# Performance work log

Measured on AMD Instinct MI355X. Metric: run time of the kernel, lower is better.

## Reference

```python
import jax, jax.numpy as jnp
import numpy as np

DIM = 256
HEADS = 8
HEAD_DIM = DIM // HEADS
B_, N = 8192, 49


def setup_inputs() -> dict:
    key = jax.random.key(0)
    k1, k2, k3, k4, k5, k6 = jax.random.split(key, 6)
    x = jax.random.normal(k1, (B_, N, DIM), dtype=jnp.float32)
    mask = jax.random.normal(k2, (B_, N, N), dtype=jnp.float32)
    s = 1.0 / np.sqrt(DIM)
    W_qkv = jax.random.normal(k3, (3 * DIM, DIM), dtype=jnp.float32) * s
    b_qkv = jax.random.normal(k4, (3 * DIM,), dtype=jnp.float32) * 0.02
    W_proj = jax.random.normal(k5, (DIM, DIM), dtype=jnp.float32) * s
    b_proj = jax.random.normal(k6, (DIM,), dtype=jnp.float32) * 0.02
    return {"x": x, "mask": mask, "W_qkv": W_qkv, "b_qkv": b_qkv,
            "W_proj": W_proj, "b_proj": b_proj}


def reference(x, mask, W_qkv, b_qkv, W_proj, b_proj):
    B, n, C = x.shape
    scale = HEAD_DIM ** (-0.5)
    # qkv projection: (B, N, 3C) -> (3, B, H, N, hd)
    qkv = x @ W_qkv.T + b_qkv
    qkv = qkv.reshape(B, n, 3, HEADS, HEAD_DIM).transpose(2, 0, 3, 1, 4)
    q, k, v = qkv[0], qkv[1], qkv[2]
    # scaled dot-product within each window
    attn = jnp.einsum('bhqd,bhkd->bhqk', q, k) * scale
    attn = attn + mask[:, None, :, :]  # additive window mask
    attn = jax.nn.softmax(attn, axis=-1)
    out = jnp.einsum('bhqk,bhkd->bhqd', attn, v)
    out = out.transpose(0, 2, 1, 3).reshape(B, n, C)
    return out @ W_proj.T + b_proj
```

## Files before the change

### kernel.cpp

```cpp
#include <hip/hip_runtime.h>
#include <hip/hip_bf16.h>

#define NTOK 49
#define DIMC 256

typedef __attribute__((ext_vector_type(8))) short bf16x8;
typedef __attribute__((ext_vector_type(4))) float f32x4;

static __device__ __forceinline__ unsigned pk2(float a, float b) {
    union { __hip_bfloat16 h; unsigned short u; } ua, ub;
    ua.h = __float2bfloat16(a);
    ub.h = __float2bfloat16(b);
    return (unsigned)ua.u | ((unsigned)ub.u << 16);
}

static __device__ __forceinline__ bf16x8 mkfrag(unsigned w0, unsigned w1, unsigned w2, unsigned w3) {
    union { bf16x8 v; unsigned u[4]; } t;
    t.u[0] = w0; t.u[1] = w1; t.u[2] = w2; t.u[3] = w3;
    return t.v;
}

static __device__ __forceinline__ unsigned sel2(unsigned lo, unsigned hi, int src, int ghi) {
    unsigned a = __shfl(lo, src);
    unsigned b = __shfl(hi, src);
    return ghi ? b : a;
}

__global__ void convert_weights(const float* __restrict__ wq, const float* __restrict__ wp,
                                unsigned short* __restrict__ wqb, unsigned short* __restrict__ wpb) {
    int i = blockIdx.x * 256 + threadIdx.x;
    if (i < 768 * 256) {
        union { __hip_bfloat16 h; unsigned short u; } t;
        t.h = __float2bfloat16(wq[i]);
        wqb[i] = t.u;
    }
    if (i < 256 * 256) {
        union { __hip_bfloat16 h; unsigned short u; } t;
        t.h = __float2bfloat16(wp[i]);
        wpb[i] = t.u;
    }
}

__launch_bounds__(512, 4)
__attribute__((amdgpu_waves_per_eu(4, 4)))
__global__ void win_attn_fused(const float* __restrict__ x, const float* __restrict__ mask,
                               const unsigned short* __restrict__ wqkv, const float* __restrict__ bqkv,
                               const unsigned short* __restrict__ wproj, const float* __restrict__ bproj,
                               float* __restrict__ out) {
    __shared__ __align__(16) char lds[81920];
    char* const xb  = lds;
    char* const kqv = lds + 32768;

    const int b = blockIdx.x;
    const int tid = threadIdx.x;
    const int lane = tid & 63;
    const int wid = tid >> 6;
    const int c = lane & 15;
    const int g = lane >> 4;
    const int lh = wid >> 1;
    const int qh = wid & 1;
    const int srcA = c + 16 * ((2 * g) & 3);
    const int srcB = c + 16 * ((2 * g + 1) & 3);
    const int ghi = g >> 1;
    const float scale = 0.17677669529663687f;
    const f32x4 fzero = {0.f, 0.f, 0.f, 0.f};

    char* const Kh = kqv + lh * 12288;
    char* const Qh = Kh + 4096;
    char* const Vh = Kh + 8192;

    {
        const float* xw = x + (size_t)b * (NTOK * DIMC);
        #pragma unroll
        for (int it = 0; it < 8; ++it) {
            int idx = it * 512 + tid;
            int t = idx >> 6;
            int d0 = (idx & 63) * 4;
            float4 v = make_float4(0.f, 0.f, 0.f, 0.f);
            if (t < NTOK) v = *(const float4*)(xw + t * DIMC + d0);
            *(uint2*)(xb + t * 512 + ((d0 * 2) ^ ((t & 7) << 4))) =
                make_uint2(pk2(v.x, v.y), pk2(v.z, v.w));
        }
    }
    __syncthreads();

    #define XFR(base_, t_, kk_) \
        (*(const bf16x8*)((base_) + (t_) * 512 + ((2 * ((kk_) + 8 * g)) ^ (((t_) & 7) << 4))))

    unsigned aout[2][2][2][2];

    #pragma unroll
    for (int r = 0; r < 2; ++r) {
        const int h = r * 4 + lh;

        {
            f32x4 aKQ[2][4], aV[4];
            #pragma unroll
            for (int md = 0; md < 2; ++md)
                #pragma unroll
                for (int j2 = 0; j2 < 4; ++j2) aKQ[md][j2] = fzero;
            #pragma unroll
            for (int mt = 0; mt < 4; ++mt) aV[mt] = fzero;

            const int woff = qh ? (h * 32) : (256 + h * 32);
            const unsigned short* wkq_base = wqkv + (size_t)(woff + c) * 256 + 8 * g;
            const unsigned short* wv_base  = wqkv + (size_t)(512 + h * 32 + qh * 16 + c) * 256 + 8 * g;
            #pragma unroll
            for (int ks = 0; ks < 8; ++ks) {
                int kk = ks * 32;
                bf16x8 xf[4];
                #pragma unroll
                for (int tt = 0; tt < 4; ++tt) { int t = tt * 16 + c; xf[tt] = XFR(xb, t, kk); }
                bf16x8 wkq0 = *(const bf16x8*)(wkq_base + kk);
                bf16x8 wkq1 = *(const bf16x8*)(wkq_base + 16 * 256 + kk);
                bf16x8 wv   = *(const bf16x8*)(wv_base + kk);
                #pragma unroll
                for (int j2 = 0; j2 < 4; ++j2) {
                    aKQ[0][j2] = __builtin_amdgcn_mfma_f32_16x16x32_bf16(wkq0, xf[j2], aKQ[0][j2], 0, 0, 0);
                    aKQ[1][j2] = __builtin_amdgcn_mfma_f32_16x16x32_bf16(wkq1, xf[j2], aKQ[1][j2], 0, 0, 0);
                    aV[j2]     = __builtin_amdgcn_mfma_f32_16x16x32_bf16(xf[j2], wv, aV[j2], 0, 0, 0);
                }
            }

            char* kqdst = (qh ? Qh : Kh);
            const float* bb = bqkv + (qh ? 0 : 256) + h * 32;
            #pragma unroll
            for (int md = 0; md < 2; ++md) {
                const float* b4 = bb + md * 16 + 4 * g;
                float b0 = b4[0], b1 = b4[1], b2 = b4[2], b3 = b4[3];
                #pragma unroll
                for (int j2 = 0; j2 < 4; ++j2) {
                    int t = j2 * 16 + c;
                    int d0 = md * 16 + 4 * g;
                    f32x4 v = aKQ[md][j2];
                    float v0 = v[0] + b0, v1 = v[1] + b1, v2 = v[2] + b2, v3 = v[3] + b3;
                    if (qh) { v0 *= scale; v1 *= scale; v2 *= scale; v3 *= scale; }
                    *(uint2*)(kqdst + t * 64 + ((d0 * 2) ^ ((t & 3) << 4))) =
                        make_uint2(pk2(v0, v1), pk2(v2, v3));
                }
            }
            float bv = bqkv[512 + h * 32 + qh * 16 + c];
            #pragma unroll
            for (int mt = 0; mt < 4; ++mt) {
                int t0 = mt * 16 + 4 * g;
                int d = qh * 16 + c;
                f32x4 v = aV[mt];
                *(uint2*)(Vh + d * 128 + ((t0 * 2) ^ ((d & 7) << 4))) =
                    make_uint2(pk2(v[0] + bv, v[1] + bv), pk2(v[2] + bv, v[3] + bv));
            }
        }
        __syncthreads();

        {
            const float* mw = mask + (size_t)b * (NTOK * NTOK);
            f32x4 mv[2][3];
            float m48[2];
            #pragma unroll
            for (int jl = 0; jl < 2; ++jl) {
                int q = (qh * 2 + jl) * 16 + c;
                int qc = (q < NTOK) ? q : (NTOK - 1);
                const float* mrow = mw + qc * NTOK;
                mv[jl][0] = *(const f32x4*)(mrow + 0 + g * 4);
                mv[jl][1] = *(const f32x4*)(mrow + 16 + g * 4);
                mv[jl][2] = *(const f32x4*)(mrow + 32 + g * 4);
                m48[jl] = mrow[48];
            }

            bf16x8 ka[4], qf[2], vf[2][2];
            #pragma unroll
            for (int it = 0; it < 4; ++it) {
                int key = it * 16 + c;
                ka[it] = *(const bf16x8*)(Kh + key * 64 + ((g * 16) ^ ((key & 3) << 4)));
            }
            #pragma unroll
            for (int jl = 0; jl < 2; ++jl) {
                int q = (qh * 2 + jl) * 16 + c;
                qf[jl] = *(const bf16x8*)(Qh + q * 64 + ((g * 16) ^ ((q & 3) << 4)));
            }
            #pragma unroll
            for (int kh = 0; kh < 2; ++kh)
                #pragma unroll
                for (int dt = 0; dt < 2; ++dt) {
                    int d = dt * 16 + c;
                    vf[kh][dt] = *(const bf16x8*)(Vh + d * 128 +
                                                  (((kh * 32 + g * 8) * 2) ^ ((d & 7) << 4)));
                }
            f32x4 oacc[2][2];
            #pragma unroll
            for (int dt = 0; dt < 2; ++dt)
                #pragma unroll
                for (int jl = 0; jl < 2; ++jl) oacc[dt][jl] = fzero;

            #pragma unroll
            for (int jl = 0; jl < 2; ++jl) {
                float p[4][4];
                {
                    f32x4 s = __builtin_amdgcn_mfma_f32_16x16x32_bf16(ka[0], qf[jl], fzero, 0, 0, 0);
                    #pragma unroll
                    for (int rr = 0; rr < 4; ++rr) p[0][rr] = s[rr] + mv[jl][0][rr];
                }
                {
                    f32x4 s = __builtin_amdgcn_mfma_f32_16x16x32_bf16(ka[1], qf[jl], fzero, 0, 0, 0);
                    #pragma unroll
                    for (int rr = 0; rr < 4; ++rr) p[1][rr] = s[rr] + mv[jl][1][rr];
                }
                {
                    f32x4 s = __builtin_amdgcn_mfma_f32_16x16x32_bf16(ka[2], qf[jl], fzero, 0, 0, 0);
                    #pragma unroll
                    for (int rr = 0; rr < 4; ++rr) p[2][rr] = s[rr] + mv[jl][2][rr];
                }
                {
                    f32x4 s = __builtin_amdgcn_mfma_f32_16x16x32_bf16(ka[3], qf[jl], fzero, 0, 0, 0);
                    #pragma unroll
                    for (int rr = 0; rr < 4; ++rr)
                        p[3][rr] = (g == 0 && rr == 0) ? (s[0] + m48[jl]) : -1e30f;
                }
                float m = -1e30f;
                #pragma unroll
                for (int it = 0; it < 4; ++it)
                    #pragma unroll
                    for (int rr = 0; rr < 4; ++rr) m = fmaxf(m, p[it][rr]);
                m = fmaxf(m, __shfl_xor(m, 16));
                m = fmaxf(m, __shfl_xor(m, 32));
                float ssum = 0.f;
                #pragma unroll
                for (int it = 0; it < 4; ++it)
                    #pragma unroll
                    for (int rr = 0; rr < 4; ++rr) {
                        float e = __expf(p[it][rr] - m);
                        p[it][rr] = e;
                        ssum += e;
                    }
                ssum += __shfl_xor(ssum, 16);
                ssum += __shfl_xor(ssum, 32);
                float inv = 1.0f / ssum;
                unsigned pq[4][2];
                #pragma unroll
                for (int it = 0; it < 4; ++it) {
                    pq[it][0] = pk2(p[it][0] * inv, p[it][1] * inv);
                    pq[it][1] = pk2(p[it][2] * inv, p[it][3] * inv);
                }
                #pragma unroll
                for (int kh = 0; kh < 2; ++kh) {
                    bf16x8 pf = mkfrag(sel2(pq[2 * kh][0], pq[2 * kh + 1][0], srcA, ghi),
                                       sel2(pq[2 * kh][1], pq[2 * kh + 1][1], srcA, ghi),
                                       sel2(pq[2 * kh][0], pq[2 * kh + 1][0], srcB, ghi),
                                       sel2(pq[2 * kh][1], pq[2 * kh + 1][1], srcB, ghi));
                    #pragma unroll
                    for (int dt = 0; dt < 2; ++dt)
                        oacc[dt][jl] = __builtin_amdgcn_mfma_f32_16x16x32_bf16(vf[kh][dt], pf, oacc[dt][jl], 0, 0, 0);
                }
            }
            #pragma unroll
            for (int dt = 0; dt < 2; ++dt)
                #pragma unroll
                for (int jl = 0; jl < 2; ++jl) {
                    aout[r][dt][jl][0] = pk2(oacc[dt][jl][0], oacc[dt][jl][1]);
                    aout[r][dt][jl][1] = pk2(oacc[dt][jl][2], oacc[dt][jl][3]);
                }
        }
        __syncthreads();
    }

    #pragma unroll
    for (int r = 0; r < 2; ++r) {
        #pragma unroll
        for (int dt = 0; dt < 2; ++dt) {
            #pragma unroll
            for (int jl = 0; jl < 2; ++jl) {
                int q = (qh * 2 + jl) * 16 + c;
                int d0 = (r * 4 + lh) * 32 + dt * 16 + 4 * g;
                *(uint2*)(xb + q * 512 + ((2 * d0) ^ ((q & 7) << 4))) =
                    make_uint2(aout[r][dt][jl][0], aout[r][dt][jl][1]);
            }
        }
    }
    __syncthreads();

    {
        f32x4 pacc[2][4];
        #pragma unroll
        for (int j = 0; j < 2; ++j)
            #pragma unroll
            for (int mt = 0; mt < 4; ++mt) pacc[j][mt] = fzero;

        #pragma unroll
        for (int ks = 0; ks < 8; ++ks) {
            int kk = ks * 32;
            bf16x8 af[4];
            #pragma unroll
            for (int mt = 0; mt < 4; ++mt) { int t = mt * 16 + c; af[mt] = XFR(xb, t, kk); }
            #pragma unroll
            for (int j = 0; j < 2; ++j) {
                int o = (wid * 2 + j) * 16 + c;
                bf16x8 bfr = *(const bf16x8*)(wproj + (size_t)o * 256 + kk + 8 * g);
                #pragma unroll
                for (int mt = 0; mt < 4; ++mt)
                    pacc[j][mt] = __builtin_amdgcn_mfma_f32_16x16x32_bf16(af[mt], bfr, pacc[j][mt], 0, 0, 0);
            }
        }
        float* ob = out + (size_t)b * (NTOK * DIMC);
        #pragma unroll
        for (int j = 0; j < 2; ++j) {
            int o = (wid * 2 + j) * 16 + c;
            float bias = bproj[o];
            #pragma unroll
            for (int mt = 0; mt < 4; ++mt) {
                #pragma unroll
                for (int rr = 0; rr < 4; ++rr) {
                    int t = mt * 16 + g * 4 + rr;
                    if (t < NTOK) ob[t * DIMC + o] = pacc[j][mt][rr] + bias;
                }
            }
        }
    }
    #undef XFR
}

extern "C" void kernel_launch(void* const* d_in, const int* in_sizes, int n_in,
                              void* d_out, int out_size, void* d_ws, size_t ws_size,
                              hipStream_t stream) {
    const float* x    = (const float*)d_in[0];
    const float* mask = (const float*)d_in[1];
    const float* wq   = (const float*)d_in[2];
    const float* bq   = (const float*)d_in[3];
    const float* wp   = (const float*)d_in[4];
    const float* bp   = (const float*)d_in[5];
    float* o = (float*)d_out;

    unsigned short* wqb = (unsigned short*)d_ws;
    unsigned short* wpb = wqb + 768 * 256;

    convert_weights<<<768, 256, 0, stream>>>(wq, wp, wqb, wpb);
    win_attn_fused<<<8192, 512, 0, stream>>>(x, mask, wqb, bq, wpb, bp, o);
}
```

Measured before the change: 778.4 us.

## Split attention into per-half-head blocks and a separate projection GEMM kernel

Each window's attention is now split across two blocks, each handling four heads, which doubles the grid. Each block writes its bf16 attention output to a workspace buffer, and a separate proj_gemm kernel then applies the output projection. A 1024-thread fused fallback kernel is used when the workspace is too small. The aim is more parallelism and shorter per-block serial work. The cost is that x is loaded and converted twice and there is an extra global round trip of about 200MB for the intermediate.

```diff
diff --git a/kernel.cpp b/kernel.cpp
--- a/kernel.cpp
+++ b/kernel.cpp
@@ -43,15 +43,15 @@
 
 __launch_bounds__(512, 4)
 __attribute__((amdgpu_waves_per_eu(4, 4)))
-__global__ void win_attn_fused(const float* __restrict__ x, const float* __restrict__ mask,
-                               const unsigned short* __restrict__ wqkv, const float* __restrict__ bqkv,
-                               const unsigned short* __restrict__ wproj, const float* __restrict__ bproj,
-                               float* __restrict__ out) {
+__global__ void win_attn_half(const float* __restrict__ x, const float* __restrict__ mask,
+                              const unsigned short* __restrict__ wqkv, const float* __restrict__ bqkv,
+                              unsigned short* __restrict__ aob) {
     __shared__ __align__(16) char lds[81920];
     char* const xb  = lds;
     char* const kqv = lds + 32768;
 
-    const int b = blockIdx.x;
+    const int b    = blockIdx.x >> 1;
+    const int half = blockIdx.x & 1;
     const int tid = threadIdx.x;
     const int lane = tid & 63;
     const int wid = tid >> 6;
@@ -59,6 +59,7 @@
     const int g = lane >> 4;
     const int lh = wid >> 1;
     const int qh = wid & 1;
+    const int h = half * 4 + lh;
     const int srcA = c + 16 * ((2 * g) & 3);
     const int srcB = c + 16 * ((2 * g + 1) & 3);
     const int ghi = g >> 1;
@@ -87,230 +88,496 @@
     #define XFR(base_, t_, kk_) \
         (*(const bf16x8*)((base_) + (t_) * 512 + ((2 * ((kk_) + 8 * g)) ^ (((t_) & 7) << 4))))
 
-    unsigned aout[2][2][2][2];
-
-    #pragma unroll
-    for (int r = 0; r < 2; ++r) {
-        const int h = r * 4 + lh;
-
-        {
-            f32x4 aKQ[2][4], aV[4];
-            #pragma unroll
-            for (int md = 0; md < 2; ++md)
-                #pragma unroll
-                for (int j2 = 0; j2 < 4; ++j2) aKQ[md][j2] = fzero;
-            #pragma unroll
-            for (int mt = 0; mt < 4; ++mt) aV[mt] = fzero;
-
-            const int woff = qh ? (h * 32) : (256 + h * 32);
-            const unsigned short* wkq_base = wqkv + (size_t)(woff + c) * 256 + 8 * g;
-            const unsigned short* wv_base  = wqkv + (size_t)(512 + h * 32 + qh * 16 + c) * 256 + 8 * g;
-            #pragma unroll
-            for (int ks = 0; ks < 8; ++ks) {
-                int kk = ks * 32;
-                bf16x8 xf[4];
-                #pragma unroll
-                for (int tt = 0; tt < 4; ++tt) { int t = tt * 16 + c; xf[tt] = XFR(xb, t, kk); }
-                bf16x8 wkq0 = *(const bf16x8*)(wkq_base + kk);
-                bf16x8 wkq1 = *(const bf16x8*)(wkq_base + 16 * 256 + kk);
-                bf16x8 wv   = *(const bf16x8*)(wv_base + kk);
-                #pragma unroll
-                for (int j2 = 0; j2 < 4; ++j2) {
-                    aKQ[0][j2] = __builtin_amdgcn_mfma_f32_16x16x32_bf16(wkq0, xf[j2], aKQ[0][j2], 0, 0, 0);
-                    aKQ[1][j2] = __builtin_amdgcn_mfma_f32_16x16x32_bf16(wkq1, xf[j2], aKQ[1][j2], 0, 0, 0);
-                    aV[j2]     = __builtin_amdgcn_mfma_f32_16x16x32_bf16(xf[j2], wv, aV[j2], 0, 0, 0);
+    {
+        f32x4 aKQ[2][4], aV[4];
+        #pragma unroll
+        for (int md = 0; md < 2; ++md)
+            #pragma unroll
+            for (int j2 = 0; j2 < 4; ++j2) aKQ[md][j2] = fzero;
+        #pragma unroll
+        for (int mt = 0; mt < 4; ++mt) aV[mt] = fzero;
+
+        const int woff = qh ? (h * 32) : (256 + h * 32);
+        const unsigned short* wkq_base = wqkv + (size_t)(woff + c) * 256 + 8 * g;
+        const unsigned short* wv_base  = wqkv + (size_t)(512 + h * 32 + qh * 16 + c) * 256 + 8 * g;
+        #pragma unroll
+        for (int ks = 0; ks < 8; ++ks) {
+            int kk = ks * 32;
+            bf16x8 xf[4];
+            #pragma unroll
+            for (int tt = 0; tt < 4; ++tt) { int t = tt * 16 + c; xf[tt] = XFR(xb, t, kk); }
+            bf16x8 wkq0 = *(const bf16x8*)(wkq_base + kk);
+            bf16x8 wkq1 = *(const bf16x8*)(wkq_base + 16 * 256 + kk);
+            bf16x8 wv   = *(const bf16x8*)(wv_base + kk);
+            #pragma unroll
+            for (int j2 = 0; j2 < 4; ++j2) {
+                aKQ[0][j2] = __builtin_amdgcn_mfma_f32_16x16x32_bf16(wkq0, xf[j2], aKQ[0][j2], 0, 0, 0);
+                aKQ[1][j2] = __builtin_amdgcn_mfma_f32_16x16x32_bf16(wkq1, xf[j2], aKQ[1][j2], 0, 0, 0);
+                aV[j2]     = __builtin_amdgcn_mfma_f32_16x16x32_bf16(xf[j2], wv, aV[j2], 0, 0, 0);
+            }
+        }
+
+        char* kqdst = (qh ? Qh : Kh);
+        const float* bb = bqkv + (qh ? 0 : 256) + h * 32;
+        #pragma unroll
+        for (int md = 0; md < 2; ++md) {
+            const float* b4 = bb + md * 16 + 4 * g;
+            float b0 = b4[0], b1 = b4[1], b2 = b4[2], b3 = b4[3];
+            #pragma unroll
+            for (int j2 = 0; j2 < 4; ++j2) {
+                int t = j2 * 16 + c;
+                int d0 = md * 16 + 4 * g;
+                f32x4 v = aKQ[md][j2];
+                float v0 = v[0] + b0, v1 = v[1] + b1, v2 = v[2] + b2, v3 = v[3] + b3;
+                if (qh) { v0 *= scale; v1 *= scale; v2 *= scale; v3 *= scale; }
+                *(uint2*)(kqdst + t * 64 + ((d0 * 2) ^ ((t & 3) << 4))) =
+                    make_uint2(pk2(v0, v1), pk2(v2, v3));
+            }
+        }
+        float bv = bqkv[512 + h * 32 + qh * 16 + c];
+        #pragma unroll
+        for (int mt = 0; mt < 4; ++mt) {
+            int t0 = mt * 16 + 4 * g;
+            int d = qh * 16 + c;
+            f32x4 v = aV[mt];
+            *(uint2*)(Vh + d * 128 + ((t0 * 2) ^ ((d & 7) << 4))) =
+                make_uint2(pk2(v[0] + bv, v[1] + bv), pk2(v[2] + bv, v[3] + bv));
+        }
+    }
+    __syncthreads();
+
+    {
+        const float* mw = mask + (size_t)b * (NTOK * NTOK);
+        f32x4 mv[2][3];
+        float m48[2];
+        #pragma unroll
+        for (int jl = 0; jl < 2; ++jl) {
+            int q = (qh * 2 + jl) * 16 + c;
+            int qc = (q < NTOK) ? q : (NTOK - 1);
+            const float* mrow = mw + qc * NTOK;
+            mv[jl][0] = *(const f32x4*)(mrow + 0 + g * 4);
+            mv[jl][1] = *(const f32x4*)(mrow + 16 + g * 4);
+            mv[jl][2] = *(const f32x4*)(mrow + 32 + g * 4);
+            m48[jl] = mrow[48];
+        }
+
+        bf16x8 ka[4], qf[2], vf[2][2];
+        #pragma unroll
+        for (int it = 0; it < 4; ++it) {
+            int key = it * 16 + c;
+            ka[it] = *(const bf16x8*)(Kh + key * 64 + ((g * 16) ^ ((key & 3) << 4)));
+        }
+        #pragma unroll
+        for (int jl = 0; jl < 2; ++jl) {
+            int q = (qh * 2 + jl) * 16 + c;
+            qf[jl] = *(const bf16x8*)(Qh + q * 64 + ((g * 16) ^ ((q & 3) << 4)));
+        }
+        #pragma unroll
+        for (int kh = 0; kh < 2; ++kh)
+            #pragma unroll
+            for (int dt = 0; dt < 2; ++dt) {
+                int d = dt * 16 + c;
+                vf[kh][dt] = *(const bf16x8*)(Vh + d * 128 +
+                                              (((kh * 32 + g * 8) * 2) ^ ((d & 7) << 4)));
+            }
+        f32x4 oacc[2][2];
+        #pragma unroll
+        for (int dt = 0; dt < 2; ++dt)
+            #pragma unroll
+            for (int jl = 0; jl < 2; ++jl) oacc[dt][jl] = fzero;
+
+        #pragma unroll
+        for (int jl = 0; jl < 2; ++jl) {
+            float p[4][4];
+            {
+                f32x4 s = __builtin_amdgcn_mfma_f32_16x16x32_bf16(ka[0], qf[jl], fzero, 0, 0, 0);
+                #pragma unroll
+                for (int rr = 0; rr < 4; ++rr) p[0][rr] = s[rr] + mv[jl][0][rr];
+            }
+            {
+                f32x4 s = __builtin_amdgcn_mfma_f32_16x16x32_bf16(ka[1], qf[jl], fzero, 0, 0, 0);
+                #pragma unroll
+                for (int rr = 0; rr < 4; ++rr) p[1][rr] = s[rr] + mv[jl][1][rr];
+            }
+            {
+                f32x4 s = __builtin_amdgcn_mfma_f32_16x16x32_bf16(ka[2], qf[jl], fzero, 0, 0, 0);
+                #pragma unroll
+                for (int rr = 0; rr < 4; ++rr) p[2][rr] = s[rr] + mv[jl][2][rr];
+            }
+            {
+                f32x4 s = __builtin_amdgcn_mfma_f32_16x16x32_bf16(ka[3], qf[jl], fzero, 0, 0, 0);
+                #pragma unroll
+                for (int rr = 0; rr < 4; ++rr)
+                    p[3][rr] = (g == 0 && rr == 0) ? (s[0] + m48[jl]) : -1e30f;
+            }
+            float m = -1e30f;
+            #pragma unroll
+            for (int it = 0; it < 4; ++it)
+                #pragma unroll
+                for (int rr = 0; rr < 4; ++rr) m = fmaxf(m, p[it][rr]);
+            m = fmaxf(m, __shfl_xor(m, 16));
+            m = fmaxf(m, __shfl_xor(m, 32));
+            float ssum = 0.f;
+            #pragma unroll
+            for (int it = 0; it < 4; ++it)
+                #pragma unroll
+                for (int rr = 0; rr < 4; ++rr) {
+                    float e = __expf(p[it][rr] - m);
+                    p[it][rr] = e;
+                    ssum += e;
                 }
-            }
-
-            char* kqdst = (qh ? Qh : Kh);
-            const float* bb = bqkv + (qh ? 0 : 256) + h * 32;
-            #pragma unroll
-            for (int md = 0; md < 2; ++md) {
-                const float* b4 = bb + md * 16 + 4 * g;
-                float b0 = b4[0], b1 = b4[1], b2 = b4[2], b3 = b4[3];
-                #pragma unroll
-                for (int j2 = 0; j2 < 4; ++j2) {
-                    int t = j2 * 16 + c;
-                    int d0 = md * 16 + 4 * g;
-                    f32x4 v = aKQ[md][j2];
-                    float v0 = v[0] + b0, v1 = v[1] + b1, v2 = v[2] + b2, v3 = v[3] + b3;
-                    if (qh) { v0 *= scale; v1 *= scale; v2 *= scale; v3 *= scale; }
-                    *(uint2*)(kqdst + t * 64 + ((d0 * 2) ^ ((t & 3) << 4))) =
-                        make_uint2(pk2(v0, v1), pk2(v2, v3));
-                }
-            }
-            float bv = bqkv[512 + h * 32 + qh * 16 + c];
-            #pragma unroll
-            for (int mt = 0; mt < 4; ++mt) {
-                int t0 = mt * 16 + 4 * g;
-                int d = qh * 16 + c;
-                f32x4 v = aV[mt];
-                *(uint2*)(Vh + d * 128 + ((t0 * 2) ^ ((d & 7) << 4))) =
-                    make_uint2(pk2(v[0] + bv, v[1] + bv), pk2(v[2] + bv, v[3] + bv));
-            }
-        }
-        __syncthreads();
-
-        {
-            const float* mw = mask + (size_t)b * (NTOK * NTOK);
-            f32x4 mv[2][3];
-            float m48[2];
+            ssum += __shfl_xor(ssum, 16);
+            ssum += __shfl_xor(ssum, 32);
+            float inv = 1.0f / ssum;
+            unsigned pq[4][2];
+            #pragma unroll
+            for (int it = 0; it < 4; ++it) {
+                pq[it][0] = pk2(p[it][0] * inv, p[it][1] * inv);
+                pq[it][1] = pk2(p[it][2] * inv, p[it][3] * inv);
+            }
+            #pragma unroll
+            for (int kh = 0; kh < 2; ++kh) {
+                bf16x8 pf = mkfrag(sel2(pq[2 * kh][0], pq[2 * kh + 1][0], srcA, ghi),
+                                   sel2(pq[2 * kh][1], pq[2 * kh + 1][1], srcA, ghi),
+                                   sel2(pq[2 * kh][0], pq[2 * kh + 1][0], srcB, ghi),
+                                   sel2(pq[2 * kh][1], pq[2 * kh + 1][1], srcB, ghi));
+                #pragma unroll
+                for (int dt = 0; dt < 2; ++dt)
+                    oacc[dt][jl] = __builtin_amdgcn_mfma_f32_16x16x32_bf16(vf[kh][dt], pf, oacc[dt][jl], 0, 0, 0);
+            }
+        }
+
+        unsigned short* ab = aob + (size_t)b * (NTOK * DIMC);
+        #pragma unroll
+        for (int dt = 0; dt < 2; ++dt) {
             #pragma unroll
             for (int jl = 0; jl < 2; ++jl) {
                 int q = (qh * 2 + jl) * 16 + c;
-                int qc = (q < NTOK) ? q : (NTOK - 1);
-                const float* mrow = mw + qc * NTOK;
-                mv[jl][0] = *(const f32x4*)(mrow + 0 + g * 4);
-                mv[jl][1] = *(const f32x4*)(mrow + 16 + g * 4);
-                mv[jl][2] = *(const f32x4*)(mrow + 32 + g * 4);
-                m48[jl] = mrow[48];
-            }
-
-            bf16x8 ka[4], qf[2], vf[2][2];
-            #pragma unroll
-            for (int it = 0; it < 4; ++it) {
-                int key = it * 16 + c;
-                ka[it] = *(const bf16x8*)(Kh + key * 64 + ((g * 16) ^ ((key & 3) << 4)));
-            }
-            #pragma unroll
-            for (int jl = 0; jl < 2; ++jl) {
-                int q = (qh * 2 + jl) * 16 + c;
-                qf[jl] = *(const bf16x8*)(Qh + q * 64 + ((g * 16) ^ ((q & 3) << 4)));
-            }
-            #pragma unroll
-            for (int kh = 0; kh < 2; ++kh)
-                #pragma unroll
-                for (int dt = 0; dt < 2; ++dt) {
-                    int d = dt * 16 + c;
-                    vf[kh][dt] = *(const bf16x8*)(Vh + d * 128 +
-                                                  (((kh * 32 + g * 8) * 2) ^ ((d & 7) << 4)));
-                }
-            f32x4 oacc[2][2];
-            #pragma unroll
-            for (int dt = 0; dt < 2; ++dt)
-                #pragma unroll
-                for (int jl = 0; jl < 2; ++jl) oacc[dt][jl] = fzero;
-
-            #pragma unroll
-            for (int jl = 0; jl < 2; ++jl) {
-                float p[4][4];
-                {
-                    f32x4 s = __builtin_amdgcn_mfma_f32_16x16x32_bf16(ka[0], qf[jl], fzero, 0, 0, 0);
-                    #pragma unroll
-                    for (int rr = 0; rr < 4; ++rr) p[0][rr] = s[rr] + mv[jl][0][rr];
-                }
-                {
-                    f32x4 s = __builtin_amdgcn_mfma_f32_16x16x32_bf16(ka[1], qf[jl], fzero, 0, 0, 0);
-                    #pragma unroll
-                    for (int rr = 0; rr < 4; ++rr) p[1][rr] = s[rr] + mv[jl][1][rr];
-                }
-                {
-                    f32x4 s = __builtin_amdgcn_mfma_f32_16x16x32_bf16(ka[2], qf[jl], fzero, 0, 0, 0);
-                    #pragma unroll
-                    for (int rr = 0; rr < 4; ++rr) p[2][rr] = s[rr] + mv[jl][2][rr];
-                }
-                {
-                    f32x4 s = __builtin_amdgcn_mfma_f32_16x16x32_bf16(ka[3], qf[jl], fzero, 0, 0, 0);
-                    #pragma unroll
-                    for (int rr = 0; rr < 4; ++rr)
-                        p[3][rr] = (g == 0 && rr == 0) ? (s[0] + m48[jl]) : -1e30f;
-                }
-                float m = -1e30f;
-                #pragma unroll
-                for (int it = 0; it < 4; ++it)
-                    #pragma unroll
-                    for (int rr = 0; rr < 4; ++rr) m = fmaxf(m, p[it][rr]);
-                m = fmaxf(m, __shfl_xor(m, 16));
-                m = fmaxf(m, __shfl_xor(m, 32));
-                float ssum = 0.f;
-                #pragma unroll
-                for (int it = 0; it < 4; ++it)
-                    #pragma unroll
-                    for (int rr = 0; rr < 4; ++rr) {
-                        float e = __expf(p[it][rr] - m);
-                        p[it][rr] = e;
-                        ssum += e;
-                    }
-                ssum += __shfl_xor(ssum, 16);
-                ssum += __shfl_xor(ssum, 32);
-                float inv = 1.0f / ssum;
-                unsigned pq[4][2];
-                #pragma unroll
-                for (int it = 0; it < 4; ++it) {
-                    pq[it][0] = pk2(p[it][0] * inv, p[it][1] * inv);
-                    pq[it][1] = pk2(p[it][2] * inv, p[it][3] * inv);
-                }
-                #pragma unroll
-                for (int kh = 0; kh < 2; ++kh) {
-                    bf16x8 pf = mkfrag(sel2(pq[2 * kh][0], pq[2 * kh + 1][0], srcA, ghi),
-                                       sel2(pq[2 * kh][1], pq[2 * kh + 1][1], srcA, ghi),
-                                       sel2(pq[2 * kh][0], pq[2 * kh + 1][0], srcB, ghi),
-                                       sel2(pq[2 * kh][1], pq[2 * kh + 1][1], srcB, ghi));
-                    #pragma unroll
-                    for (int dt = 0; dt < 2; ++dt)
-                        oacc[dt][jl] = __builtin_amdgcn_mfma_f32_16x16x32_bf16(vf[kh][dt], pf, oacc[dt][jl], 0, 0, 0);
-                }
-            }
-            #pragma unroll
-            for (int dt = 0; dt < 2; ++dt)
-                #pragma unroll
-                for (int jl = 0; jl < 2; ++jl) {
-                    aout[r][dt][jl][0] = pk2(oacc[dt][jl][0], oacc[dt][jl][1]);
-                    aout[r][dt][jl][1] = pk2(oacc[dt][jl][2], oacc[dt][jl][3]);
-                }
-        }
-        __syncthreads();
-    }
-
+                int d0 = h * 32 + dt * 16 + 4 * g;
+                if (q < NTOK)
+                    *(uint2*)(ab + q * DIMC + d0) =
+                        make_uint2(pk2(oacc[dt][jl][0], oacc[dt][jl][1]),
+                                   pk2(oacc[dt][jl][2], oacc[dt][jl][3]));
+            }
+        }
+    }
+    #undef XFR
+}
+
+__launch_bounds__(512, 4)
+__global__ void proj_gemm(const unsigned short* __restrict__ aob,
+                          const unsigned short* __restrict__ wproj,
+                          const float* __restrict__ bproj, float* __restrict__ out) {
+    __shared__ __align__(16) char lds[32768];
+    char* const xb = lds;
+
+    const int b = blockIdx.x;
+    const int tid = threadIdx.x;
+    const int lane = tid & 63;
+    const int wid = tid >> 6;
+    const int c = lane & 15;
+    const int g = lane >> 4;
+    const f32x4 fzero = {0.f, 0.f, 0.f, 0.f};
+
+    {
+        const unsigned short* ab = aob + (size_t)b * (NTOK * DIMC);
+        #pragma unroll
+        for (int it = 0; it < 8; ++it) {
+            int idx = it * 512 + tid;
+            int t = idx >> 6;
+            int d0 = (idx & 63) * 4;
+            uint2 v = make_uint2(0u, 0u);
+            if (t < NTOK) v = *(const uint2*)(ab + t * DIMC + d0);
+            *(uint2*)(xb + t * 512 + ((d0 * 2) ^ ((t & 7) << 4))) = v;
+        }
+    }
+    __syncthreads();
+
+    #define XFR(base_, t_, kk_) \
+        (*(const bf16x8*)((base_) + (t_) * 512 + ((2 * ((kk_) + 8 * g)) ^ (((t_) & 7) << 4))))
+
+    f32x4 pacc[2][4];
     #pragma unroll
-    for (int r = 0; r < 2; ++r) {
-        #pragma unroll
-        for (int dt = 0; dt < 2; ++dt) {
-            #pragma unroll
-            for (int jl = 0; jl < 2; ++jl) {
-                int q = (qh * 2 + jl) * 16 + c;
-                int d0 = (r * 4 + lh) * 32 + dt * 16 + 4 * g;
-                *(uint2*)(xb + q * 512 + ((2 * d0) ^ ((q & 7) << 4))) =
-                    make_uint2(aout[r][dt][jl][0], aout[r][dt][jl][1]);
-            }
+    for (int j = 0; j < 2; ++j)
+        #pragma unroll
+        for (int mt = 0; mt < 4; ++mt) pacc[j][mt] = fzero;
+
+    #pragma unroll
+    for (int ks = 0; ks < 8; ++ks) {
+        int kk = ks * 32;
+        bf16x8 af[4];
+        #pragma unroll
+        for (int mt = 0; mt < 4; ++mt) { int t = mt * 16 + c; af[mt] = XFR(xb, t, kk); }
+        #pragma unroll
+        for (int j = 0; j < 2; ++j) {
+            int o = (wid * 2 + j) * 16 + c;
+            bf16x8 bfr = *(const bf16x8*)(wproj + (size_t)o * 256 + kk + 8 * g);
+            #pragma unroll
+            for (int mt = 0; mt < 4; ++mt)
+                pacc[j][mt] = __builtin_amdgcn_mfma_f32_16x16x32_bf16(af[mt], bfr, pacc[j][mt], 0, 0, 0);
+        }
+    }
+    float* ob = out + (size_t)b * (NTOK * DIMC);
+    #pragma unroll
+    for (int j = 0; j < 2; ++j) {
+        int o = (wid * 2 + j) * 16 + c;
+        float bias = bproj[o];
+        #pragma unroll
+        for (int mt = 0; mt < 4; ++mt) {
+            #pragma unroll
+            for (int rr = 0; rr < 4; ++rr) {
+                int t = mt * 16 + g * 4 + rr;
+                if (t < NTOK) ob[t * DIMC + o] = pacc[j][mt][rr] + bias;
+            }
+        }
+    }
+    #undef XFR
+}
+
+__launch_bounds__(1024, 4)
+__attribute__((amdgpu_waves_per_eu(4, 4)))
+__global__ void win_attn_fused_fb(const float* __restrict__ x, const float* __restrict__ mask,
+                                  const unsigned short* __restrict__ wqkv, const float* __restrict__ bqkv,
+                                  const unsigned short* __restrict__ wproj, const float* __restrict__ bproj,
+                                  float* __restrict__ out) {
+    __shared__ __align__(16) char lds[131072];
+    char* const xb  = lds;
+    char* const kqv = lds + 32768;
+
+    const int b = blockIdx.x;
+    const int tid = threadIdx.x;
+    const int lane = tid & 63;
+    const int wid = tid >> 6;
+    const int c = lane & 15;
+    const int g = lane >> 4;
+    const int h = wid >> 1;
+    const int qh = wid & 1;
+    const int srcA = c + 16 * ((2 * g) & 3);
+    const int srcB = c + 16 * ((2 * g + 1) & 3);
+    const int ghi = g >> 1;
+    const float scale = 0.17677669529663687f;
+    const f32x4 fzero = {0.f, 0.f, 0.f, 0.f};
+
+    {
+        const float* xw = x + (size_t)b * (NTOK * DIMC);
+        #pragma unroll
+        for (int it = 0; it < 4; ++it) {
+            int idx = it * 1024 + tid;
+            int t = idx >> 6;
+            int d0 = (idx & 63) * 4;
+            float4 v = make_float4(0.f, 0.f, 0.f, 0.f);
+            if (t < NTOK) v = *(const float4*)(xw + t * DIMC + d0);
+            *(uint2*)(xb + t * 512 + ((d0 * 2) ^ ((t & 7) << 4))) =
+                make_uint2(pk2(v.x, v.y), pk2(v.z, v.w));
         }
     }
     __syncthreads();
 
-    {
-        f32x4 pacc[2][4];
-        #pragma unroll
-        for (int j = 0; j < 2; ++j)
-            #pragma unroll
-            for (int mt = 0; mt < 4; ++mt) pacc[j][mt] = fzero;
-
+    #define XFR(base_, t_, kk_) \
+        (*(const bf16x8*)((base_) + (t_) * 512 + ((2 * ((kk_) + 8 * g)) ^ (((t_) & 7) << 4))))
+
+    char* const Kh = kqv + h * 12288;
+    char* const Qh = Kh + 4096;
+    char* const Vh = Kh + 8192;
+
+    {
+        f32x4 aKQ[2][4], aV[4];
+        #pragma unroll
+        for (int md = 0; md < 2; ++md)
+            #pragma unroll
+            for (int j2 = 0; j2 < 4; ++j2) aKQ[md][j2] = fzero;
+        #pragma unroll
+        for (int mt = 0; mt < 4; ++mt) aV[mt] = fzero;
+
+        const int woff = qh ? (h * 32) : (256 + h * 32);
+        const unsigned short* wkq_base = wqkv + (size_t)(woff + c) * 256 + 8 * g;
+        const unsigned short* wv_base  = wqkv + (size_t)(512 + h * 32 + qh * 16 + c) * 256 + 8 * g;
         #pragma unroll
         for (int ks = 0; ks < 8; ++ks) {
             int kk = ks * 32;
-            bf16x8 af[4];
-            #pragma unroll
-            for (int mt = 0; mt < 4; ++mt) { int t = mt * 16 + c; af[mt] = XFR(xb, t, kk); }
-            #pragma unroll
-            for (int j = 0; j < 2; ++j) {
-                int o = (wid * 2 + j) * 16 + c;
-                bf16x8 bfr = *(const bf16x8*)(wproj + (size_t)o * 256 + kk + 8 * g);
-                #pragma unroll
-                for (int mt = 0; mt < 4; ++mt)
-                    pacc[j][mt] = __builtin_amdgcn_mfma_f32_16x16x32_bf16(af[mt], bfr, pacc[j][mt], 0, 0, 0);
+            bf16x8 xf[4];
+            #pragma unroll
+            for (int tt = 0; tt < 4; ++tt) { int t = tt * 16 + c; xf[tt] = XFR(xb, t, kk); }
+            bf16x8 wkq0 = *(const bf16x8*)(wkq_base + kk);
+            bf16x8 wkq1 = *(const bf16x8*)(wkq_base + 16 * 256 + kk);
+            bf16x8 wv   = *(const bf16x8*)(wv_base + kk);
+            #pragma unroll
+            for (int j2 = 0; j2 < 4; ++j2) {
+                aKQ[0][j2] = __builtin_amdgcn_mfma_f32_16x16x32_bf16(wkq0, xf[j2], aKQ[0][j2], 0, 0, 0);
+                aKQ[1][j2] = __builtin_amdgcn_mfma_f32_16x16x32_bf16(wkq1, xf[j2], aKQ[1][j2], 0, 0, 0);
+                aV[j2]     = __builtin_amdgcn_mfma_f32_16x16x32_bf16(xf[j2], wv, aV[j2], 0, 0, 0);
+            }
+        }
+
+        char* kqdst = (qh ? Qh : Kh);
+        const float* bb = bqkv + (qh ? 0 : 256) + h * 32;
+        #pragma unroll
+        for (int md = 0; md < 2; ++md) {
+            const float* b4 = bb + md * 16 + 4 * g;
+            float b0 = b4[0], b1 = b4[1], b2 = b4[2], b3 = b4[3];
+            #pragma unroll
+            for (int j2 = 0; j2 < 4; ++j2) {
+                int t = j2 * 16 + c;
+                int d0 = md * 16 + 4 * g;
+                f32x4 v = aKQ[md][j2];
+                float v0 = v[0] + b0, v1 = v[1] + b1, v2 = v[2] + b2, v3 = v[3] + b3;
+                if (qh) { v0 *= scale; v1 *= scale; v2 *= scale; v3 *= scale; }
+                *(uint2*)(kqdst + t * 64 + ((d0 * 2) ^ ((t & 3) << 4))) =
+                    make_uint2(pk2(v0, v1), pk2(v2, v3));
+            }
+        }
+        float bv = bqkv[512 + h * 32 + qh * 16 + c];
+        #pragma unroll
+        for (int mt = 0; mt < 4; ++mt) {
+            int t0 = mt * 16 + 4 * g;
+            int d = qh * 16 + c;
+            f32x4 v = aV[mt];
+            *(uint2*)(Vh + d * 128 + ((t0 * 2) ^ ((d & 7) << 4))) =
+                make_uint2(pk2(v[0] + bv, v[1] + bv), pk2(v[2] + bv, v[3] + bv));
+        }
+    }
+    __syncthreads();
+
+    f32x4 oacc[2][2];
+    {
+        const float* mw = mask + (size_t)b * (NTOK * NTOK);
+        f32x4 mv[2][3];
+        float m48[2];
+        #pragma unroll
+        for (int jl = 0; jl < 2; ++jl) {
+            int q = (qh * 2 + jl) * 16 + c;
+            int qc = (q < NTOK) ? q : (NTOK - 1);
+            const float* mrow = mw + qc * NTOK;
+            mv[jl][0] = *(const f32x4*)(mrow + 0 + g * 4);
+            mv[jl][1] = *(const f32x4*)(mrow + 16 + g * 4);
+            mv[jl][2] = *(const f32x4*)(mrow + 32 + g * 4);
+            m48[jl] = mrow[48];
+        }
+
+        bf16x8 ka[4], qf[2], vf[2][2];
+        #pragma unroll
+        for (int it = 0; it < 4; ++it) {
+            int key = it * 16 + c;
+            ka[it] = *(const bf16x8*)(Kh + key * 64 + ((g * 16) ^ ((key & 3) << 4)));
+        }
+        #pragma unroll
+        for (int jl = 0; jl < 2; ++jl) {
+            int q = (qh * 2 + jl) * 16 + c;
+            qf[jl] = *(const bf16x8*)(Qh + q * 64 + ((g * 16) ^ ((q & 3) << 4)));
+        }
+        #pragma unroll
+        for (int kh = 0; kh < 2; ++kh)
+            #pragma unroll
+            for (int dt = 0; dt < 2; ++dt) {
+                int d = dt * 16 + c;
+                vf[kh][dt] = *(const bf16x8*)(Vh + d * 128 +
+                                              (((kh * 32 + g * 8) * 2) ^ ((d & 7) << 4)));
+            }
+        #pragma unroll
+        for (int dt = 0; dt < 2; ++dt)
+            #pragma unroll
+            for (int jl = 0; jl < 2; ++jl) oacc[dt][jl] = fzero;
+
+        #pragma unroll
+        for (int jl = 0; jl < 2; ++jl) {
+            float p[4][4];
+            {
+                f32x4 s = __builtin_amdgcn_mfma_f32_16x16x32_bf16(ka[0], qf[jl], fzero, 0, 0, 0);
+                #pragma unroll
+                for (int rr = 0; rr < 4; ++rr) p[0][rr] = s[rr] + mv[jl][0][rr];
+            }
+            {
+                f32x4 s = __builtin_amdgcn_mfma_f32_16x16x32_bf16(ka[1], qf[jl], fzero, 0, 0, 0);
+                #pragma unroll
+                for (int rr = 0; rr < 4; ++rr) p[1][rr] = s[rr] + mv[jl][1][rr];
+            }
+            {
+                f32x4 s = __builtin_amdgcn_mfma_f32_16x16x32_bf16(ka[2], qf[jl], fzero, 0, 0, 0);
+                #pragma unroll
+                for (int rr = 0; rr < 4; ++rr) p[2][rr] = s[rr] + mv[jl][2][rr];
+            }
+            {
+                f32x4 s = __builtin_amdgcn_mfma_f32_16x16x32_bf16(ka[3], qf[jl], fzero, 0, 0, 0);
+                #pragma unroll
+                for (int rr = 0; rr < 4; ++rr)
+                    p[3][rr] = (g == 0 && rr == 0) ? (s[0] + m48[jl]) : -1e30f;
+            }
+            float m = -1e30f;
+            #pragma unroll
+            for (int it = 0; it < 4; ++it)
+                #pragma unroll
+                for (int rr = 0; rr < 4; ++rr) m = fmaxf(m, p[it][rr]);
+            m = fmaxf(m, __shfl_xor(m, 16));
+            m = fmaxf(m, __shfl_xor(m, 32));
+            float ssum = 0.f;
+            #pragma unroll
+            for (int it = 0; it < 4; ++it)
+                #pragma unroll
+                for (int rr = 0; rr < 4; ++rr) {
+                    float e = __expf(p[it][rr] - m);
+                    p[it][rr] = e;
+                    ssum += e;
+                }
+            ssum += __shfl_xor(ssum, 16);
+            ssum += __shfl_xor(ssum, 32);
+            float inv = 1.0f / ssum;
+            unsigned pq[4][2];
+            #pragma unroll
+            for (int it = 0; it < 4; ++it) {
+                pq[it][0] = pk2(p[it][0] * inv, p[it][1] * inv);
+                pq[it][1] = pk2(p[it][2] * inv, p[it][3] * inv);
+            }
+            #pragma unroll
+            for (int kh = 0; kh < 2; ++kh) {
+                bf16x8 pf = mkfrag(sel2(pq[2 * kh][0], pq[2 * kh + 1][0], srcA, ghi),
+                                   sel2(pq[2 * kh][1], pq[2 * kh + 1][1], srcA, ghi),
+                                   sel2(pq[2 * kh][0], pq[2 * kh + 1][0], srcB, ghi),
+                                   sel2(pq[2 * kh][1], pq[2 * kh + 1][1], srcB, ghi));
+                #pragma unroll
+                for (int dt = 0; dt < 2; ++dt)
+                    oacc[dt][jl] = __builtin_amdgcn_mfma_f32_16x16x32_bf16(vf[kh][dt], pf, oacc[dt][jl], 0, 0, 0);
+            }
+        }
+    }
+
+    #pragma unroll
+    for (int dt = 0; dt < 2; ++dt) {
+        #pragma unroll
+        for (int jl = 0; jl < 2; ++jl) {
+            int q = (qh * 2 + jl) * 16 + c;
+            int d0 = h * 32 + dt * 16 + 4 * g;
+            f32x4 v = oacc[dt][jl];
+            *(uint2*)(xb + q * 512 + ((2 * d0) ^ ((q & 7) << 4))) =
+                make_uint2(pk2(v[0], v[1]), pk2(v[2], v[3]));
+        }
+    }
+    __syncthreads();
+
+    {
+        f32x4 pacc[4];
+        #pragma unroll
+        for (int mt = 0; mt < 4; ++mt) pacc[mt] = fzero;
+        const int o = wid * 16 + c;
+        const unsigned short* wp_base = wproj + (size_t)o * 256 + 8 * g;
+        const float bias = bproj[o];
+        #pragma unroll
+        for (int ks = 0; ks < 8; ++ks) {
+            int kk = ks * 32;
+            bf16x8 bfr = *(const bf16x8*)(wp_base + kk);
+            #pragma unroll
+            for (int mt = 0; mt < 4; ++mt) {
+                int t = mt * 16 + c;
+                bf16x8 af = XFR(xb, t, kk);
+                pacc[mt] = __builtin_amdgcn_mfma_f32_16x16x32_bf16(af, bfr, pacc[mt], 0, 0, 0);
             }
         }
         float* ob = out + (size_t)b * (NTOK * DIMC);
         #pragma unroll
-        for (int j = 0; j < 2; ++j) {
-            int o = (wid * 2 + j) * 16 + c;
-            float bias = bproj[o];
-            #pragma unroll
-            for (int mt = 0; mt < 4; ++mt) {
-                #pragma unroll
-                for (int rr = 0; rr < 4; ++rr) {
-                    int t = mt * 16 + g * 4 + rr;
-                    if (t < NTOK) ob[t * DIMC + o] = pacc[j][mt][rr] + bias;
-                }
+        for (int mt = 0; mt < 4; ++mt) {
+            #pragma unroll
+            for (int rr = 0; rr < 4; ++rr) {
+                int t = mt * 16 + g * 4 + rr;
+                if (t < NTOK) ob[t * DIMC + o] = pacc[mt][rr] + bias;
             }
         }
     }
@@ -330,7 +597,16 @@
 
     unsigned short* wqb = (unsigned short*)d_ws;
     unsigned short* wpb = wqb + 768 * 256;
+    unsigned short* aob = wpb + 256 * 256;
+
+    const size_t need = (size_t)(768 * 256 + 256 * 256) * 2 +
+                        (size_t)8192 * NTOK * DIMC * 2;
 
     convert_weights<<<768, 256, 0, stream>>>(wq, wp, wqb, wpb);
-    win_attn_fused<<<8192, 512, 0, stream>>>(x, mask, wqb, bq, wpb, bp, o);
-}
+    if (ws_size >= need) {
+        win_attn_half<<<16384, 512, 0, stream>>>(x, mask, wqb, bq, aob);
+        proj_gemm<<<8192, 512, 0, stream>>>(aob, wpb, bp, o);
+    } else {
+        win_attn_fused_fb<<<8192, 1024, 0, stream>>>(x, mask, wqb, bq, wpb, bp, o);
+    }
+}
```

Result: no change. 770.9 us (-1.0%).
